# Performance work log

Hardware: AMD Instinct MI355X
Metric: run time of the kernel (lower is better)

## Reference

```python
import jax, jax.numpy as jnp
import numpy as np

NUM_SEGMENTS = 256
HIDDEN = 512
N_NODES = 100000


def setup_inputs() -> dict:
    key = jax.random.key(0)
    k_x, k_b, k_w, k_bias = jax.random.split(key, 4)
    x = jax.random.normal(k_x, (N_NODES, HIDDEN), dtype=jnp.float32)
    batch = jnp.sort(jax.random.randint(k_b, (N_NODES,), 0, NUM_SEGMENTS, dtype=jnp.int64))
    # gate_nn = Linear(hidden_size, 1)
    bound = 1.0 / np.sqrt(HIDDEN)
    W = jax.random.uniform(k_w, (HIDDEN, 1), dtype=jnp.float32, minval=-bound, maxval=bound)
    b = jax.random.uniform(k_bias, (1,), dtype=jnp.float32, minval=-bound, maxval=bound)
    return {"x": x, "batch": batch, "W": W, "b": b}


def reference(x, batch, W, b):
    # gate = gate_nn(x) -> [N, 1]
    gate = (x @ W + b)[:, 0]  # [N]
    # segment-wise numerically-stable softmax over nodes of each graph
    gmax = jax.ops.segment_max(gate, batch, num_segments=NUM_SEGMENTS)  # [B]
    e = jnp.exp(gate - gmax[batch])  # [N]
    denom = jax.ops.segment_sum(e, batch, num_segments=NUM_SEGMENTS)  # [B]
    alpha = e / (denom[batch] + 1e-16)  # [N]
    # weighted scatter-sum pooling: out[b] = sum_{i in b} alpha_i * x_i
    out = jax.ops.segment_sum(alpha[:, None] * x, batch, num_segments=NUM_SEGMENTS)  # [B, H]
    return out
```

## Files before the change

kernel.cpp:

```cpp
#include <hip/hip_runtime.h>

#define N_SEG 256
#define HIDDEN 512
#define CHUNKS 8
#define NEG_INF (-__builtin_inff())

__global__ void bounds_kernel(const int* __restrict__ batch, int* __restrict__ seg_off, int n) {
    int s = blockIdx.x * blockDim.x + threadIdx.x;
    if (s > N_SEG) return;
    int lo = 0, hi = n;
    while (lo < hi) { int mid = (lo + hi) >> 1; if (batch[mid] < s) lo = mid + 1; else hi = mid; }
    seg_off[s] = lo;
}

__global__ __launch_bounds__(256) void fused_kernel(
    const float* __restrict__ x, const float* __restrict__ W,
    const int* __restrict__ seg_off,
    float* __restrict__ pm, float* __restrict__ pd, float* __restrict__ pacc) {
    int s = blockIdx.x >> 3, c = blockIdx.x & 7;
    int t = threadIdx.x, lane = t & 63, w = t >> 6;
    int ss = seg_off[s], se = seg_off[s + 1];
    int len = se - ss;
    int i0 = ss + (int)(((long long)len * c) >> 3);
    int i1 = ss + (int)(((long long)len * (c + 1)) >> 3);
    int pidx = blockIdx.x;

    if (i0 >= i1) {
        if (t == 0) { pm[pidx] = NEG_INF; pd[pidx] = 0.0f; }
        for (int j = t; j < HIDDEN; j += 256) pacc[(size_t)pidx * HIDDEN + j] = 0.0f;
        return;
    }

    float4 w0 = *(const float4*)(W + lane * 8);
    float4 w1 = *(const float4*)(W + lane * 8 + 4);
    float m = NEG_INF, d = 0.0f;
    float acc[8] = {0, 0, 0, 0, 0, 0, 0, 0};

    int i = i0 + w;
    bool have = i < i1;
    float4 a0, a1;
    if (have) {
        const float* xr = x + (size_t)i * HIDDEN + lane * 8;
        a0 = *(const float4*)xr; a1 = *(const float4*)(xr + 4);
    }
    while (have) {
        int inext = i + 4;
        bool hnext = inext < i1;
        float4 b0, b1;
        if (hnext) {
            const float* xr = x + (size_t)inext * HIDDEN + lane * 8;
            b0 = *(const float4*)xr; b1 = *(const float4*)(xr + 4);
        }
        float g = a0.x * w0.x + a0.y * w0.y + a0.z * w0.z + a0.w * w0.w
                + a1.x * w1.x + a1.y * w1.y + a1.z * w1.z + a1.w * w1.w;
        #pragma unroll
        for (int off = 32; off; off >>= 1) g += __shfl_xor(g, off, 64);
        float mn = fmaxf(m, g);
        float scale = __expf(m - mn);
        float p = __expf(g - mn);
        d = d * scale + p;
        acc[0] = acc[0] * scale + p * a0.x;  acc[1] = acc[1] * scale + p * a0.y;
        acc[2] = acc[2] * scale + p * a0.z;  acc[3] = acc[3] * scale + p * a0.w;
        acc[4] = acc[4] * scale + p * a1.x;  acc[5] = acc[5] * scale + p * a1.y;
        acc[6] = acc[6] * scale + p * a1.z;  acc[7] = acc[7] * scale + p * a1.w;
        m = mn;
        a0 = b0; a1 = b1; i = inext; have = hnext;
    }

    __shared__ float sm[4], sd[4];
    __shared__ float sacc[4][HIDDEN];
    if (lane == 0) sm[w] = m;
    __syncthreads();
    float M = fmaxf(fmaxf(sm[0], sm[1]), fmaxf(sm[2], sm[3]));
    float scale = (m == NEG_INF) ? 0.0f : __expf(m - M);
    if (lane == 0) sd[w] = d * scale;
    #pragma unroll
    for (int j = 0; j < 8; ++j) sacc[w][lane * 8 + j] = acc[j] * scale;
    __syncthreads();
    if (t == 0) { pm[pidx] = M; pd[pidx] = sd[0] + sd[1] + sd[2] + sd[3]; }
    for (int j = t; j < HIDDEN; j += 256)
        pacc[(size_t)pidx * HIDDEN + j] = sacc[0][j] + sacc[1][j] + sacc[2][j] + sacc[3][j];
}

__global__ __launch_bounds__(256) void merge_kernel(
    const float* __restrict__ pm, const float* __restrict__ pd,
    const float* __restrict__ pacc, float* __restrict__ out) {
    int s = blockIdx.x, t = threadIdx.x;
    float M = NEG_INF;
    #pragma unroll
    for (int c = 0; c < CHUNKS; ++c) M = fmaxf(M, pm[s * CHUNKS + c]);
    float wts[CHUNKS];
    float D = 0.0f;
    #pragma unroll
    for (int c = 0; c < CHUNKS; ++c) {
        float mc = pm[s * CHUNKS + c];
        float wc = (mc == NEG_INF) ? 0.0f : __expf(mc - M);
        wts[c] = wc;
        D += pd[s * CHUNKS + c] * wc;
    }
    float invD = 1.0f / (D + 1e-16f);
    #pragma unroll
    for (int rep = 0; rep < 2; ++rep) {
        int j = t + rep * 256;
        float num = 0.0f;
        #pragma unroll
        for (int c = 0; c < CHUNKS; ++c)
            num += pacc[((size_t)(s * CHUNKS + c)) * HIDDEN + j] * wts[c];
        out[s * HIDDEN + j] = num * invD;
    }
}

extern "C" void kernel_launch(void* const* d_in, const int* in_sizes, int n_in,
                              void* d_out, int out_size, void* d_ws, size_t ws_size,
                              hipStream_t stream) {
    const float* x     = (const float*)d_in[0];
    const int*   batch = (const int*)d_in[1];
    const float* W     = (const float*)d_in[2];
    int n = in_sizes[1];
    float* out = (float*)d_out;

    float* pm   = (float*)d_ws;
    float* pd   = pm + N_SEG * CHUNKS;
    float* pacc = pd + N_SEG * CHUNKS;
    int* seg_off = (int*)(pacc + (size_t)N_SEG * CHUNKS * HIDDEN);

    bounds_kernel<<<2, 256, 0, stream>>>(batch, seg_off, n);
    fused_kernel<<<N_SEG * CHUNKS, 256, 0, stream>>>(x, W, seg_off, pm, pd, pacc);
    merge_kernel<<<N_SEG, 256, 0, stream>>>(pm, pd, pacc, out);
}
```

Before: 47.09 us.

## Split segments into fixed-size row chunks with prefix-sum block mapping

Replaces the fixed 8-chunks-per-segment split with a variable number of blocks per segment, each covering up to 32 rows. The block-to-segment map is built by a prefix sum in the bounds kernel. The goal is to balance work across blocks and raise the block count, so each block handles a short contiguous run and more memory parallelism is exposed. The cost is more partial accumulators to write and merge (about 3400 blocks versus 2048), a serial merge loop with an exp per partial for each column, and a single-block bounds kernel that now does the scan.

```diff
diff --git a/kernel.cpp b/kernel.cpp
--- a/kernel.cpp
+++ b/kernel.cpp
@@ -2,42 +2,55 @@
 
 #define N_SEG 256
 #define HIDDEN 512
-#define CHUNKS 8
+#define CL 32
 #define NEG_INF (-__builtin_inff())
 
-__global__ void bounds_kernel(const int* __restrict__ batch, int* __restrict__ seg_off, int n) {
-    int s = blockIdx.x * blockDim.x + threadIdx.x;
-    if (s > N_SEG) return;
-    int lo = 0, hi = n;
-    while (lo < hi) { int mid = (lo + hi) >> 1; if (batch[mid] < s) lo = mid + 1; else hi = mid; }
-    seg_off[s] = lo;
+__global__ __launch_bounds__(256) void bounds_kernel(
+    const int* __restrict__ batch, int* __restrict__ seg_off,
+    int* __restrict__ blockbase, int n) {
+    __shared__ int soff[N_SEG + 1];
+    __shared__ int sc[N_SEG];
+    int t = threadIdx.x;
+    for (int sid = t; sid <= N_SEG; sid += 256) {
+        int lo = 0, hi = n;
+        while (lo < hi) { int mid = (lo + hi) >> 1; if (batch[mid] < sid) lo = mid + 1; else hi = mid; }
+        soff[sid] = lo;
+        seg_off[sid] = lo;
+    }
+    __syncthreads();
+    sc[t] = (soff[t + 1] - soff[t] + CL - 1) / CL;
+    __syncthreads();
+    for (int off = 1; off < N_SEG; off <<= 1) {
+        int v = (t >= off) ? sc[t - off] : 0;
+        __syncthreads();
+        sc[t] += v;
+        __syncthreads();
+    }
+    blockbase[t + 1] = sc[t];
+    if (t == 0) blockbase[0] = 0;
 }
 
 __global__ __launch_bounds__(256) void fused_kernel(
     const float* __restrict__ x, const float* __restrict__ W,
-    const int* __restrict__ seg_off,
-    float* __restrict__ pm, float* __restrict__ pd, float* __restrict__ pacc) {
-    int s = blockIdx.x >> 3, c = blockIdx.x & 7;
+    const int* __restrict__ seg_off, const int* __restrict__ blockbase,
+    float* __restrict__ pacc, float* __restrict__ pm, float* __restrict__ pd) {
+    int b = blockIdx.x;
+    if (b >= blockbase[N_SEG]) return;
+    int lo = 0, hi = N_SEG;
+    while (hi - lo > 1) { int mid = (lo + hi) >> 1; if (blockbase[mid] <= b) lo = mid; else hi = mid; }
+    int s = lo;
+    int ss = seg_off[s], se = seg_off[s + 1];
+    int st = ss + (b - blockbase[s]) * CL;
+    int en = st + CL < se ? st + CL : se;
+
     int t = threadIdx.x, lane = t & 63, w = t >> 6;
-    int ss = seg_off[s], se = seg_off[s + 1];
-    int len = se - ss;
-    int i0 = ss + (int)(((long long)len * c) >> 3);
-    int i1 = ss + (int)(((long long)len * (c + 1)) >> 3);
-    int pidx = blockIdx.x;
-
-    if (i0 >= i1) {
-        if (t == 0) { pm[pidx] = NEG_INF; pd[pidx] = 0.0f; }
-        for (int j = t; j < HIDDEN; j += 256) pacc[(size_t)pidx * HIDDEN + j] = 0.0f;
-        return;
-    }
-
     float4 w0 = *(const float4*)(W + lane * 8);
     float4 w1 = *(const float4*)(W + lane * 8 + 4);
     float m = NEG_INF, d = 0.0f;
     float acc[8] = {0, 0, 0, 0, 0, 0, 0, 0};
 
-    int i = i0 + w;
-    bool have = i < i1;
+    int i = st + w;
+    bool have = i < en;
     float4 a0, a1;
     if (have) {
         const float* xr = x + (size_t)i * HIDDEN + lane * 8;
@@ -45,7 +58,7 @@
     }
     while (have) {
         int inext = i + 4;
-        bool hnext = inext < i1;
+        bool hnext = inext < en;
         float4 b0, b1;
         if (hnext) {
             const float* xr = x + (size_t)inext * HIDDEN + lane * 8;
@@ -77,36 +90,29 @@
     #pragma unroll
     for (int j = 0; j < 8; ++j) sacc[w][lane * 8 + j] = acc[j] * scale;
     __syncthreads();
-    if (t == 0) { pm[pidx] = M; pd[pidx] = sd[0] + sd[1] + sd[2] + sd[3]; }
+    if (t == 0) { pm[b] = M; pd[b] = sd[0] + sd[1] + sd[2] + sd[3]; }
     for (int j = t; j < HIDDEN; j += 256)
-        pacc[(size_t)pidx * HIDDEN + j] = sacc[0][j] + sacc[1][j] + sacc[2][j] + sacc[3][j];
+        pacc[(size_t)b * HIDDEN + j] = sacc[0][j] + sacc[1][j] + sacc[2][j] + sacc[3][j];
 }
 
 __global__ __launch_bounds__(256) void merge_kernel(
+    const int* __restrict__ blockbase, const float* __restrict__ pacc,
     const float* __restrict__ pm, const float* __restrict__ pd,
-    const float* __restrict__ pacc, float* __restrict__ out) {
+    float* __restrict__ out) {
     int s = blockIdx.x, t = threadIdx.x;
+    int k0 = blockbase[s], k1 = blockbase[s + 1];
     float M = NEG_INF;
-    #pragma unroll
-    for (int c = 0; c < CHUNKS; ++c) M = fmaxf(M, pm[s * CHUNKS + c]);
-    float wts[CHUNKS];
+    for (int k = k0; k < k1; ++k) M = fmaxf(M, pm[k]);
     float D = 0.0f;
-    #pragma unroll
-    for (int c = 0; c < CHUNKS; ++c) {
-        float mc = pm[s * CHUNKS + c];
-        float wc = (mc == NEG_INF) ? 0.0f : __expf(mc - M);
-        wts[c] = wc;
-        D += pd[s * CHUNKS + c] * wc;
-    }
+    for (int k = k0; k < k1; ++k) D += pd[k] * __expf(pm[k] - M);
     float invD = 1.0f / (D + 1e-16f);
     #pragma unroll
     for (int rep = 0; rep < 2; ++rep) {
-        int j = t + rep * 256;
+        int col = t + rep * 256;
         float num = 0.0f;
-        #pragma unroll
-        for (int c = 0; c < CHUNKS; ++c)
-            num += pacc[((size_t)(s * CHUNKS + c)) * HIDDEN + j] * wts[c];
-        out[s * HIDDEN + j] = num * invD;
+        for (int k = k0; k < k1; ++k)
+            num += pacc[(size_t)k * HIDDEN + col] * __expf(pm[k] - M);
+        out[s * HIDDEN + col] = num * invD;
     }
 }
 
@@ -119,12 +125,14 @@
     int n = in_sizes[1];
     float* out = (float*)d_out;
 
-    float* pm   = (float*)d_ws;
-    float* pd   = pm + N_SEG * CHUNKS;
-    float* pacc = pd + N_SEG * CHUNKS;
-    int* seg_off = (int*)(pacc + (size_t)N_SEG * CHUNKS * HIDDEN);
+    int nb = (n + CL - 1) / CL + N_SEG;
+    float* pacc = (float*)d_ws;
+    float* pm   = pacc + (size_t)nb * HIDDEN;
+    float* pd   = pm + nb;
+    int* seg_off   = (int*)(pd + nb);
+    int* blockbase = seg_off + (N_SEG + 1);
 
-    bounds_kernel<<<2, 256, 0, stream>>>(batch, seg_off, n);
-    fused_kernel<<<N_SEG * CHUNKS, 256, 0, stream>>>(x, W, seg_off, pm, pd, pacc);
-    merge_kernel<<<N_SEG, 256, 0, stream>>>(pm, pd, pacc, out);
+    bounds_kernel<<<1, 256, 0, stream>>>(batch, seg_off, blockbase, n);
+    fused_kernel<<<nb, 256, 0, stream>>>(x, W, seg_off, blockbase, pacc, pm, pd);
+    merge_kernel<<<N_SEG, 256, 0, stream>>>(blockbase, pacc, pm, pd, out);
 }
```

New measurement: 58.63 us. +24.5%, slower.

## Fold segment bounds search into fused kernel and double chunks per segment

Applied to the files above, without the earlier changes.

Removes the separate bounds kernel launch; every block now binary-searches the sorted batch array for its own segment start and end. The chunk count per segment goes from 8 to 16, giving 4096 blocks with fewer rows each to improve GPU occupancy and latency hiding. The trade-off is redundant binary searches across blocks and twice the partial accumulator traffic read back by the merge kernel.

```diff
diff --git a/kernel.cpp b/kernel.cpp
--- a/kernel.cpp
+++ b/kernel.cpp
@@ -2,32 +2,30 @@
 
 #define N_SEG 256
 #define HIDDEN 512
-#define CHUNKS 8
+#define CHUNKS 16
 #define NEG_INF (-__builtin_inff())
-
-__global__ void bounds_kernel(const int* __restrict__ batch, int* __restrict__ seg_off, int n) {
-    int s = blockIdx.x * blockDim.x + threadIdx.x;
-    if (s > N_SEG) return;
-    int lo = 0, hi = n;
-    while (lo < hi) { int mid = (lo + hi) >> 1; if (batch[mid] < s) lo = mid + 1; else hi = mid; }
-    seg_off[s] = lo;
-}
 
 __global__ __launch_bounds__(256) void fused_kernel(
     const float* __restrict__ x, const float* __restrict__ W,
-    const int* __restrict__ seg_off,
-    float* __restrict__ pm, float* __restrict__ pd, float* __restrict__ pacc) {
-    int s = blockIdx.x >> 3, c = blockIdx.x & 7;
+    const int* __restrict__ batch,
+    float* __restrict__ pacc, float* __restrict__ pm, float* __restrict__ pd,
+    int n) {
+    int b = blockIdx.x;
+    int s = b >> 4, c = b & 15;
     int t = threadIdx.x, lane = t & 63, w = t >> 6;
-    int ss = seg_off[s], se = seg_off[s + 1];
+
+    int lo = 0, hi = n;
+    while (lo < hi) { int mid = (lo + hi) >> 1; if (batch[mid] < s) lo = mid + 1; else hi = mid; }
+    int ss = lo; hi = n;
+    while (lo < hi) { int mid = (lo + hi) >> 1; if (batch[mid] < s + 1) lo = mid + 1; else hi = mid; }
+    int se = lo;
     int len = se - ss;
-    int i0 = ss + (int)(((long long)len * c) >> 3);
-    int i1 = ss + (int)(((long long)len * (c + 1)) >> 3);
-    int pidx = blockIdx.x;
+    int st = ss + (int)(((long long)len * c) >> 4);
+    int en = ss + (int)(((long long)len * (c + 1)) >> 4);
 
-    if (i0 >= i1) {
-        if (t == 0) { pm[pidx] = NEG_INF; pd[pidx] = 0.0f; }
-        for (int j = t; j < HIDDEN; j += 256) pacc[(size_t)pidx * HIDDEN + j] = 0.0f;
+    if (st >= en) {
+        if (t == 0) { pm[b] = NEG_INF; pd[b] = 0.0f; }
+        for (int j = t; j < HIDDEN; j += 256) pacc[(size_t)b * HIDDEN + j] = 0.0f;
         return;
     }
 
@@ -36,8 +34,8 @@
     float m = NEG_INF, d = 0.0f;
     float acc[8] = {0, 0, 0, 0, 0, 0, 0, 0};
 
-    int i = i0 + w;
-    bool have = i < i1;
+    int i = st + w;
+    bool have = i < en;
     float4 a0, a1;
     if (have) {
         const float* xr = x + (size_t)i * HIDDEN + lane * 8;
@@ -45,7 +43,7 @@
     }
     while (have) {
         int inext = i + 4;
-        bool hnext = inext < i1;
+        bool hnext = inext < en;
         float4 b0, b1;
         if (hnext) {
             const float* xr = x + (size_t)inext * HIDDEN + lane * 8;
@@ -77,36 +75,37 @@
     #pragma unroll
     for (int j = 0; j < 8; ++j) sacc[w][lane * 8 + j] = acc[j] * scale;
     __syncthreads();
-    if (t == 0) { pm[pidx] = M; pd[pidx] = sd[0] + sd[1] + sd[2] + sd[3]; }
+    if (t == 0) { pm[b] = M; pd[b] = sd[0] + sd[1] + sd[2] + sd[3]; }
     for (int j = t; j < HIDDEN; j += 256)
-        pacc[(size_t)pidx * HIDDEN + j] = sacc[0][j] + sacc[1][j] + sacc[2][j] + sacc[3][j];
+        pacc[(size_t)b * HIDDEN + j] = sacc[0][j] + sacc[1][j] + sacc[2][j] + sacc[3][j];
 }
 
 __global__ __launch_bounds__(256) void merge_kernel(
-    const float* __restrict__ pm, const float* __restrict__ pd,
-    const float* __restrict__ pacc, float* __restrict__ out) {
+    const float* __restrict__ pacc, const float* __restrict__ pm,
+    const float* __restrict__ pd, float* __restrict__ out) {
     int s = blockIdx.x, t = threadIdx.x;
+    int k0 = s * CHUNKS;
     float M = NEG_INF;
     #pragma unroll
-    for (int c = 0; c < CHUNKS; ++c) M = fmaxf(M, pm[s * CHUNKS + c]);
+    for (int k = 0; k < CHUNKS; ++k) M = fmaxf(M, pm[k0 + k]);
     float wts[CHUNKS];
     float D = 0.0f;
     #pragma unroll
-    for (int c = 0; c < CHUNKS; ++c) {
-        float mc = pm[s * CHUNKS + c];
-        float wc = (mc == NEG_INF) ? 0.0f : __expf(mc - M);
-        wts[c] = wc;
-        D += pd[s * CHUNKS + c] * wc;
+    for (int k = 0; k < CHUNKS; ++k) {
+        float mk = pm[k0 + k];
+        float wk = (mk == NEG_INF) ? 0.0f : __expf(mk - M);
+        wts[k] = wk;
+        D += pd[k0 + k] * wk;
     }
     float invD = 1.0f / (D + 1e-16f);
     #pragma unroll
     for (int rep = 0; rep < 2; ++rep) {
-        int j = t + rep * 256;
+        int col = t + rep * 256;
         float num = 0.0f;
         #pragma unroll
-        for (int c = 0; c < CHUNKS; ++c)
-            num += pacc[((size_t)(s * CHUNKS + c)) * HIDDEN + j] * wts[c];
-        out[s * HIDDEN + j] = num * invD;
+        for (int k = 0; k < CHUNKS; ++k)
+            num += pacc[(size_t)(k0 + k) * HIDDEN + col] * wts[k];
+        out[s * HIDDEN + col] = num * invD;
     }
 }
 
@@ -119,12 +118,11 @@
     int n = in_sizes[1];
     float* out = (float*)d_out;
 
-    float* pm   = (float*)d_ws;
-    float* pd   = pm + N_SEG * CHUNKS;
-    float* pacc = pd + N_SEG * CHUNKS;
-    int* seg_off = (int*)(pacc + (size_t)N_SEG * CHUNKS * HIDDEN);
+    const int nb = N_SEG * CHUNKS;
+    float* pacc = (float*)d_ws;
+    float* pm   = pacc + (size_t)nb * HIDDEN;
+    float* pd   = pm + nb;
 
-    bounds_kernel<<<2, 256, 0, stream>>>(batch, seg_off, n);
-    fused_kernel<<<N_SEG * CHUNKS, 256, 0, stream>>>(x, W, seg_off, pm, pd, pacc);
-    merge_kernel<<<N_SEG, 256, 0, stream>>>(pm, pd, pacc, out);
+    fused_kernel<<<nb, 256, 0, stream>>>(x, W, batch, pacc, pm, pd, n);
+    merge_kernel<<<N_SEG, 256, 0, stream>>>(pacc, pm, pd, out);
 }
```

Result: slower. 48.10 us (+2.1%).
